# Optimization experiments

Hardware: AMD Instinct MI355X
Metric: run time of the kernel (lower is better)

Reference implementation:

```python
import math
import jax, jax.numpy as jnp
import numpy as np

B, T, C, FD, K, V = 8, 2048, 256, 256, 128, 256

def setup_inputs() -> dict:
    key = jax.random.key(0)
    ks = jax.random.split(key, 8)
    s = 0.02
    return {
        "inp": jax.random.normal(ks[0], (B, T, C), jnp.float32),
        "feature": jax.random.normal(ks[1], (B, T, FD), jnp.float32),
        "Wq": jax.random.normal(ks[2], (C + FD, K), jnp.float32) * s,
        "bq": jnp.zeros((K,), jnp.float32),
        "Wk": jax.random.normal(ks[3], (C, K), jnp.float32) * s,
        "bk": jnp.zeros((K,), jnp.float32),
        "Wv": jax.random.normal(ks[4], (C, V), jnp.float32) * s,
        "bv": jnp.zeros((V,), jnp.float32),
    }

def reference(inp, feature, Wq, bq, Wk, bk, Wv, bv):
    # inp: [B,T,C], feature: [B,T,FD]
    t = inp.shape[1]
    q = jnp.concatenate([inp, feature], axis=-1) @ Wq + bq   # [B,T,K]
    k = inp @ Wk + bk                                        # [B,T,K]
    v = inp @ Wv + bv                                        # [B,T,V]
    # scores[b, j, i] = q_j . k_i ; original masks where i > j (strict upper tri)
    scores = jnp.einsum('bjk,bik->bji', q, k)                # [B,T,T]
    mask = jnp.triu(jnp.ones((t, t), dtype=bool), k=1)       # mask[j,i] = i > j
    scores = jnp.where(mask[None], -jnp.inf, scores) / math.sqrt(K)
    # NOTE: original softmax is over dim=1 (the query/row axis), not the key axis
    attn = jax.nn.softmax(scores, axis=1)                    # [B,T,T]
    out = jnp.einsum('bji,biv->bjv', attn, v)                # [B,T,V]
    return jnp.concatenate([inp, out], axis=-1)              # [B,T,C+V]
```

## Files before the change

### kernel.cpp

```cpp
#include <hip/hip_runtime.h>
#include <hip/hip_bf16.h>
#include <cstdint>

#define Bb  8
#define Tt  2048
#define Cc  256
#define FDd 256
#define Kk  128
#define Vv  256
#define BT  (Bb * Tt)
#define NTRI 136

#define INV_SQRT_K 0.08838834764831845f

typedef __bf16 bf16x8 __attribute__((ext_vector_type(8)));
typedef __bf16 bf16x4 __attribute__((ext_vector_type(4)));
typedef float  f32x4  __attribute__((ext_vector_type(4)));

__device__ __forceinline__ void gload16(const void* g, void* l) {
  __builtin_amdgcn_global_load_lds(
      (const __attribute__((address_space(1))) void*)g,
      (__attribute__((address_space(3))) void*)l, 16, 0, 0);
}

__global__ __launch_bounds__(256) void prepw_kernel(
    const float4* __restrict__ inp4, const float4* __restrict__ feat4,
    float4* __restrict__ out4, bf16x4* __restrict__ inpB4,
    bf16x4* __restrict__ featB4,
    const float* __restrict__ Wq, const float* __restrict__ Wk,
    const float* __restrict__ Wv, __bf16* __restrict__ Wqt,
    __bf16* __restrict__ Wkt, __bf16* __restrict__ Wvt)
{
  if (blockIdx.x < 4096) {
    const int g = blockIdx.x * 256 + threadIdx.x;
    const int row = g >> 6, c = g & 63;
    const float4 x = inp4[g];
    out4[(size_t)row * 128 + c] = x;
    bf16x4 xb; xb[0] = (__bf16)x.x; xb[1] = (__bf16)x.y; xb[2] = (__bf16)x.z; xb[3] = (__bf16)x.w;
    inpB4[g] = xb;
    const float4 f = feat4[g];
    bf16x4 fb; fb[0] = (__bf16)f.x; fb[1] = (__bf16)f.y; fb[2] = (__bf16)f.z; fb[3] = (__bf16)f.w;
    featB4[g] = fb;
  } else {
    const int g = (blockIdx.x - 4096) * 256 + threadIdx.x;
    if (g < 65536) {
      const int n = g >> 9, k = g & 511;
      Wqt[g] = (__bf16)Wq[k * 128 + n];
    } else if (g < 98304) {
      const int h = g - 65536;
      const int n = h >> 8, k = h & 255;
      Wkt[h] = (__bf16)Wk[k * 128 + n];
    } else {
      const int h = g - 98304;
      const int n = h >> 8, k = h & 255;
      Wvt[h] = (__bf16)Wv[k * 256 + n];
    }
  }
}

__global__ __launch_bounds__(256, 3) void qkv_mfma_kernel(
    const __bf16* __restrict__ inpB, const __bf16* __restrict__ featB,
    const __bf16* __restrict__ Wqt, const __bf16* __restrict__ Wkt,
    const __bf16* __restrict__ Wvt,
    const float* __restrict__ bq, const float* __restrict__ bk,
    const float* __restrict__ bv,
    __bf16* __restrict__ qb, __bf16* __restrict__ kb, __bf16* __restrict__ vT)
{
  __shared__ __bf16 Atile[128 * 64];
  __shared__ __bf16 Btile[128 * 64];
  const int panel = blockIdx.y;
  const int m0 = blockIdx.x * 128;
  const int lane = threadIdx.x & 63, wave = threadIdx.x >> 6;
  const int cl = lane & 15, quad = lane >> 4;
  const int jl0 = (wave >> 1) * 64;
  const int vl0 = (wave & 1) * 64;

  const __bf16* Wt; const float* bias; int kblocks;
  if (panel == 0)      { Wt = Wqt; bias = bq; kblocks = 8; }
  else if (panel == 1) { Wt = Wkt; bias = bk; kblocks = 4; }
  else                 { Wt = Wvt + (size_t)(panel - 2) * 128 * 256;
                         bias = bv + (panel - 2) * 128; kblocks = 4; }
  const int Kd = kblocks * 64;

  const int lrow = lane >> 3;
  const int lchunk = ((lane & 7) ^ lrow) * 8;

  f32x4 acc[4][4];
#pragma unroll
  for (int mt = 0; mt < 4; ++mt)
#pragma unroll
    for (int nt = 0; nt < 4; ++nt) acc[mt][nt] = (f32x4){0.f, 0.f, 0.f, 0.f};

  for (int kb = 0; kb < kblocks; ++kb) {
    const __bf16* Asrc = (panel == 0 && kb >= 4) ? featB : inpB;
    const int koff = (panel == 0 && kb >= 4) ? (kb - 4) * 64 : kb * 64;
    __syncthreads();
#pragma unroll
    for (int t = 0; t < 4; ++t) {
      const int r0 = wave * 32 + t * 8;
      gload16(Asrc + (size_t)(m0 + r0 + lrow) * 256 + koff + lchunk, Atile + r0 * 64);
      gload16(Wt + (size_t)(r0 + lrow) * Kd + kb * 64 + lchunk, Btile + r0 * 64);
    }
    __syncthreads();
#pragma unroll
    for (int ks = 0; ks < 2; ++ks) {
      bf16x8 af[4], bfr[4];
#pragma unroll
      for (int mt = 0; mt < 4; ++mt) {
        const int jlr = jl0 + mt * 16 + cl;
        af[mt] = *(const bf16x8*)(Atile + jlr * 64 + (((ks * 4 + quad) ^ (jlr & 7)) * 8));
      }
#pragma unroll
      for (int nt = 0; nt < 4; ++nt) {
        const int vlr = vl0 + nt * 16 + cl;
        bfr[nt] = *(const bf16x8*)(Btile + vlr * 64 + (((ks * 4 + quad) ^ (vlr & 7)) * 8));
      }
#pragma unroll
      for (int mt = 0; mt < 4; ++mt)
#pragma unroll
        for (int nt = 0; nt < 4; ++nt)
          acc[mt][nt] = __builtin_amdgcn_mfma_f32_16x16x32_bf16(af[mt], bfr[nt], acc[mt][nt], 0, 0, 0);
    }
  }

  if (panel < 2) {
    __bf16* dst = (panel == 0) ? qb : kb;
    const float scale = (panel == 0) ? INV_SQRT_K : 1.0f;
#pragma unroll
    for (int mt = 0; mt < 4; ++mt) {
      const int row = m0 + jl0 + mt * 16 + quad * 4;
#pragma unroll
      for (int nt = 0; nt < 4; ++nt) {
        const int col = vl0 + nt * 16 + cl;
        const float bs = bias[col];
#pragma unroll
        for (int r = 0; r < 4; ++r)
          dst[(size_t)(row + r) * Kk + col] = (__bf16)((acc[mt][nt][r] + bs) * scale);
      }
    }
  } else {
    const int b = m0 >> 11;
#pragma unroll
    for (int mt = 0; mt < 4; ++mt) {
      const int t0 = (m0 & (Tt - 1)) + jl0 + mt * 16 + quad * 4;
#pragma unroll
      for (int nt = 0; nt < 4; ++nt) {
        const int vcol = (panel - 2) * 128 + vl0 + nt * 16 + cl;
        const float bs = bias[vl0 + nt * 16 + cl];
        bf16x4 v4;
#pragma unroll
        for (int r = 0; r < 4; ++r) v4[r] = (__bf16)(acc[mt][nt][r] + bs);
        *(bf16x4*)(vT + (size_t)(b * Vv + vcol) * Tt + t0) = v4;
      }
    }
  }
}

__global__ __launch_bounds__(256, 2) void sexp_kernel(
    const __bf16* __restrict__ qb, const __bf16* __restrict__ kb,
    __bf16* __restrict__ expS, float* __restrict__ partialD)
{
  __shared__ __bf16 tiles[2 * 128 * 128];
  __shared__ float lcs[4][64];
  __bf16* Qtile = tiles;
  __bf16* Ktile = tiles + 128 * 128;
  float*  P     = (float*)tiles;

  const int b = blockIdx.y, l = blockIdx.x;
  int jt = 0, base = 0;
  while (base + jt + 1 <= l) { base += jt + 1; ++jt; }
  const int it = l - base;

  const int lane = threadIdx.x & 63, wave = threadIdx.x >> 6;
  const int cl = lane & 15, quad = lane >> 4;
  const int jl0 = (wave >> 1) * 64;
  const int il0 = (wave & 1) * 64;
  const size_t rowbase = (size_t)b * Tt;

  {
    const int srow = lane >> 4;
    const int cslot = lane & 15;
    const __bf16* qsrc = qb + (rowbase + jt * 128) * Kk;
    const __bf16* ksrc = kb + (rowbase + it * 128) * Kk;
#pragma unroll
    for (int t = 0; t < 8; ++t) {
      const int r0 = wave * 32 + t * 4;
      const int row = r0 + srow;
      const int cg = (cslot ^ (row & 7)) * 8;
      gload16(qsrc + (size_t)row * Kk + cg, Qtile + r0 * 128);
      gload16(ksrc + (size_t)row * Kk + cg, Ktile + r0 * 128);
    }
  }
  __syncthreads();

  f32x4 acc[4][4];
#pragma unroll
  for (int mt = 0; mt < 4; ++mt)
#pragma unroll
    for (int nt = 0; nt < 4; ++nt) acc[mt][nt] = (f32x4){0.f, 0.f, 0.f, 0.f};

#pragma unroll
  for (int s = 0; s < 4; ++s) {
    bf16x8 af[4], bfr[4];
#pragma unroll
    for (int mt = 0; mt < 4; ++mt) {
      const int jlr = jl0 + mt * 16 + cl;
      af[mt] = *(const bf16x8*)(Qtile + jlr * 128 + (((s * 4 + quad) ^ (jlr & 7)) * 8));
    }
#pragma unroll
    for (int nt = 0; nt < 4; ++nt) {
      const int ilr = il0 + nt * 16 + cl;
      bfr[nt] = *(const bf16x8*)(Ktile + ilr * 128 + (((s * 4 + quad) ^ (ilr & 7)) * 8));
    }
#pragma unroll
    for (int mt = 0; mt < 4; ++mt)
#pragma unroll
      for (int nt = 0; nt < 4; ++nt)
        acc[mt][nt] = __builtin_amdgcn_mfma_f32_16x16x32_bf16(af[mt], bfr[nt], acc[mt][nt], 0, 0, 0);
  }
  __syncthreads();

  const bool diag = (it == jt);
  float cs[4] = {0.f, 0.f, 0.f, 0.f};
#pragma unroll
  for (int mt = 0; mt < 4; ++mt) {
    const int jl = jl0 + mt * 16 + quad * 4;
#pragma unroll
    for (int nt = 0; nt < 4; ++nt) {
      const int il = il0 + nt * 16 + cl;
#pragma unroll
      for (int r = 0; r < 4; ++r) {
        float p = __expf(acc[mt][nt][r]);
        if (diag && il > (jl + r)) p = 0.f;
        cs[nt] += (float)(__bf16)p;
        P[(jl + r) * 128 + il] = p;
      }
    }
  }
#pragma unroll
  for (int nt = 0; nt < 4; ++nt) {
    cs[nt] += __shfl_xor(cs[nt], 16);
    cs[nt] += __shfl_xor(cs[nt], 32);
  }
  if (quad == 0) {
#pragma unroll
    for (int nt = 0; nt < 4; ++nt) lcs[wave][nt * 16 + cl] = cs[nt];
  }
  __syncthreads();

  __bf16* slot = expS + ((size_t)(b * NTRI + l)) * (128 * 128);
  {
    const int srow = lane >> 4;
    const int c0 = (lane & 15) * 8;
#pragma unroll
    for (int t = 0; t < 8; ++t) {
      const int row = wave * 32 + t * 4 + srow;
      const f32x4 p0 = *(const f32x4*)(P + row * 128 + c0);
      const f32x4 p1 = *(const f32x4*)(P + row * 128 + c0 + 4);
      bf16x8 pb;
#pragma unroll
      for (int u = 0; u < 4; ++u) { pb[u] = (__bf16)p0[u]; pb[4 + u] = (__bf16)p1[u]; }
      *(bf16x8*)(slot + (size_t)row * 128 + c0) = pb;
    }
  }

  const int tid = threadIdx.x;
  if (tid < 128) {
    const int w0 = (tid < 64) ? 0 : 1;
    const int lc = tid & 63;
    const float s = lcs[w0][lc] + lcs[w0 + 2][lc];
    partialD[((size_t)b * 16 + jt) * Tt + it * 128 + tid] = s;
  }
}

__global__ __launch_bounds__(256) void dvscale_kernel(
    const float* __restrict__ partialD, bf16x8* __restrict__ vT8)
{
  __shared__ float rec[32];
  const int blk = blockIdx.x;
  const int b = blk >> 6, ic = blk & 63;
  const int i0 = ic * 32;
  const int tid = threadIdx.x;
  if (tid < 32) {
    const int i = i0 + tid;
    float s = 0.f;
#pragma unroll
    for (int jt = 0; jt < 16; ++jt) s += partialD[((size_t)b * 16 + jt) * Tt + i];
    rec[tid] = 1.0f / s;
  }
  __syncthreads();
  const int iu = tid & 3, v0 = tid >> 2;
#pragma unroll
  for (int p = 0; p < 4; ++p) {
    const int v = v0 + p * 64;
    const size_t idx = ((size_t)b * Vv + v) * (Tt / 8) + (i0 >> 3) + iu;
    bf16x8 x = vT8[idx];
    const int rb = iu * 8;
#pragma unroll
    for (int t = 0; t < 8; ++t) x[t] = (__bf16)((float)x[t] * rec[rb + t]);
    vT8[idx] = x;
  }
}

__global__ __launch_bounds__(512, 2) void pvgemm_kernel(
    const __bf16* __restrict__ expS, const __bf16* __restrict__ vT,
    float* __restrict__ out)
{
  __shared__ __bf16 At[2][128 * 64];
  __shared__ __bf16 Bt[2][128 * 64];
  __shared__ float red[4][16][256];
  const int b = blockIdx.y;
  const int jt = 15 - (blockIdx.x >> 1);
  const int nh = blockIdx.x & 1;
  const int tid = (int)threadIdx.x;
  const int lane = tid & 63, wave = tid >> 6;
  const int kh = wave >> 2;
  const int sq = wave & 3;
  const int cl = lane & 15, quad = lane >> 4;
  const int jl0 = (sq >> 1) * 64;
  const int vl0 = (sq & 1) * 64;

  const int nk = (jt + 1) * 2;
  const int half = nk >> 1;
  const size_t slotbase = (size_t)(b * NTRI + (jt * (jt + 1)) / 2) * 16384;
  const __bf16* vbase = vT + ((size_t)b * Vv + nh * 128) * Tt;

  const int lrow = lane >> 3;
  const int lchunk = ((lane & 7) ^ lrow) * 8;

  f32x4 acc[4][4];
#pragma unroll
  for (int mt = 0; mt < 4; ++mt)
#pragma unroll
    for (int nt = 0; nt < 4; ++nt) acc[mt][nt] = (f32x4){0.f, 0.f, 0.f, 0.f};

  for (int kbl = 0; kbl < half; ++kbl) {
    const int kb = kh * half + kbl;
    const int i0 = kb * 64;
    const __bf16* Ag = expS + slotbase + (size_t)(kb >> 1) * 16384 + (kb & 1) * 64;
    __syncthreads();
#pragma unroll
    for (int t = 0; t < 4; ++t) {
      const int r0 = sq * 32 + t * 8;
      gload16(Ag + (size_t)(r0 + lrow) * 128 + lchunk, At[kh] + r0 * 64);
      gload16(vbase + (size_t)(r0 + lrow) * Tt + i0 + lchunk, Bt[kh] + r0 * 64);
    }
    __syncthreads();
#pragma unroll
    for (int ks = 0; ks < 2; ++ks) {
      bf16x8 af[4], bfr[4];
#pragma unroll
      for (int mt = 0; mt < 4; ++mt) {
        const int jlr = jl0 + mt * 16 + cl;
        af[mt] = *(const bf16x8*)(At[kh] + jlr * 64 + (((ks * 4 + quad) ^ (jlr & 7)) * 8));
      }
#pragma unroll
      for (int nt = 0; nt < 4; ++nt) {
        const int vlr = vl0 + nt * 16 + cl;
        bfr[nt] = *(const bf16x8*)(Bt[kh] + vlr * 64 + (((ks * 4 + quad) ^ (vlr & 7)) * 8));
      }
#pragma unroll
      for (int mt = 0; mt < 4; ++mt)
#pragma unroll
        for (int nt = 0; nt < 4; ++nt)
          acc[mt][nt] = __builtin_amdgcn_mfma_f32_16x16x32_bf16(af[mt], bfr[nt], acc[mt][nt], 0, 0, 0);
    }
  }

  __syncthreads();
  if (kh == 1) {
#pragma unroll
    for (int mt = 0; mt < 4; ++mt)
#pragma unroll
      for (int nt = 0; nt < 4; ++nt)
        *(f32x4*)&red[sq][mt * 4 + nt][lane * 4] = acc[mt][nt];
  }
  __syncthreads();
  if (kh == 0) {
#pragma unroll
    for (int mt = 0; mt < 4; ++mt)
#pragma unroll
      for (int nt = 0; nt < 4; ++nt) {
        const f32x4 o = *(const f32x4*)&red[sq][mt * 4 + nt][lane * 4];
        acc[mt][nt] += o;
      }
    float* orow = out + ((size_t)b * Tt + jt * 128 + jl0) * (size_t)(Cc + Vv)
                + Cc + nh * 128 + vl0;
#pragma unroll
    for (int mt = 0; mt < 4; ++mt)
#pragma unroll
      for (int nt = 0; nt < 4; ++nt)
#pragma unroll
        for (int r = 0; r < 4; ++r)
          orow[(size_t)(mt * 16 + quad * 4 + r) * (Cc + Vv) + nt * 16 + cl] = acc[mt][nt][r];
  }
}

extern "C" void kernel_launch(void* const* d_in, const int* in_sizes, int n_in,
                              void* d_out, int out_size, void* d_ws, size_t ws_size,
                              hipStream_t stream) {
  const float* inp  = (const float*)d_in[0];
  const float* feat = (const float*)d_in[1];
  const float* Wq   = (const float*)d_in[2];
  const float* bq   = (const float*)d_in[3];
  const float* Wk   = (const float*)d_in[4];
  const float* bk   = (const float*)d_in[5];
  const float* Wv   = (const float*)d_in[6];
  const float* bv   = (const float*)d_in[7];
  float* out = (float*)d_out;

  char* ws = (char*)d_ws;
  __bf16* inpB   = (__bf16*)(ws);
  __bf16* featB  = (__bf16*)(ws + (8u << 20));
  __bf16* qb     = (__bf16*)(ws + (16u << 20));
  __bf16* kb     = (__bf16*)(ws + (20u << 20));
  __bf16* vT     = (__bf16*)(ws + (24u << 20));
  __bf16* Wqt    = (__bf16*)(ws + (32u << 20));
  __bf16* Wkt    = (__bf16*)(ws + (32u << 20) + (128u << 10));
  __bf16* Wvt    = (__bf16*)(ws + (32u << 20) + (192u << 10));
  float*  partialD = (float*)(ws + (33u << 20));
  __bf16* expS     = (__bf16*)(ws + (36u << 20));

  prepw_kernel<<<dim3(4096 + 640), 256, 0, stream>>>(
      (const float4*)inp, (const float4*)feat, (float4*)out,
      (bf16x4*)inpB, (bf16x4*)featB, Wq, Wk, Wv, Wqt, Wkt, Wvt);
  qkv_mfma_kernel<<<dim3(BT / 128, 4), 256, 0, stream>>>(
      inpB, featB, Wqt, Wkt, Wvt, bq, bk, bv, qb, kb, vT);
  sexp_kernel<<<dim3(NTRI, Bb), 256, 0, stream>>>(qb, kb, expS, partialD);
  dvscale_kernel<<<dim3(512), 256, 0, stream>>>(partialD, (bf16x8*)vT);
  pvgemm_kernel<<<dim3(32, Bb), 512, 0, stream>>>(expS, vT, out);
}
```

Before: 170.5 us.

## Recompute attention scores in PV kernel instead of materializing exp matrix

Replaces the exp-score materialization plus V-rescale pipeline with a column-sum-only pass followed by a fused kernel that recomputes QK^T, applies exp, the causal mask and the column reciprocal, and multiplies by V through an LDS tile. This removes the large bf16 expS buffer write and read and the separate dvscale launch. In exchange it doubles the QK^T compute, loads K and V fragments directly from global memory without LDS staging, and has each block redundantly reduce partialD sums.

```diff
diff --git a/kernel.cpp b/kernel.cpp
--- a/kernel.cpp
+++ b/kernel.cpp
@@ -156,16 +156,11 @@
   }
 }
 
-__global__ __launch_bounds__(256, 2) void sexp_kernel(
-    const __bf16* __restrict__ qb, const __bf16* __restrict__ kb,
-    __bf16* __restrict__ expS, float* __restrict__ partialD)
+__global__ __launch_bounds__(256, 2) void sd_kernel(
+    const __bf16* __restrict__ qb, const __bf16* __restrict__ kbuf,
+    float* __restrict__ partialD)
 {
-  __shared__ __bf16 tiles[2 * 128 * 128];
   __shared__ float lcs[4][64];
-  __bf16* Qtile = tiles;
-  __bf16* Ktile = tiles + 128 * 128;
-  float*  P     = (float*)tiles;
-
   const int b = blockIdx.y, l = blockIdx.x;
   int jt = 0, base = 0;
   while (base + jt + 1 <= l) { base += jt + 1; ++jt; }
@@ -176,22 +171,8 @@
   const int jl0 = (wave >> 1) * 64;
   const int il0 = (wave & 1) * 64;
   const size_t rowbase = (size_t)b * Tt;
-
-  {
-    const int srow = lane >> 4;
-    const int cslot = lane & 15;
-    const __bf16* qsrc = qb + (rowbase + jt * 128) * Kk;
-    const __bf16* ksrc = kb + (rowbase + it * 128) * Kk;
-#pragma unroll
-    for (int t = 0; t < 8; ++t) {
-      const int r0 = wave * 32 + t * 4;
-      const int row = r0 + srow;
-      const int cg = (cslot ^ (row & 7)) * 8;
-      gload16(qsrc + (size_t)row * Kk + cg, Qtile + r0 * 128);
-      gload16(ksrc + (size_t)row * Kk + cg, Ktile + r0 * 128);
-    }
-  }
-  __syncthreads();
+  const __bf16* qsrc = qb + (rowbase + jt * 128) * Kk;
+  const __bf16* ksrc = kbuf + (rowbase + it * 128) * Kk;
 
   f32x4 acc[4][4];
 #pragma unroll
@@ -203,22 +184,17 @@
   for (int s = 0; s < 4; ++s) {
     bf16x8 af[4], bfr[4];
 #pragma unroll
-    for (int mt = 0; mt < 4; ++mt) {
-      const int jlr = jl0 + mt * 16 + cl;
-      af[mt] = *(const bf16x8*)(Qtile + jlr * 128 + (((s * 4 + quad) ^ (jlr & 7)) * 8));
-    }
-#pragma unroll
-    for (int nt = 0; nt < 4; ++nt) {
-      const int ilr = il0 + nt * 16 + cl;
-      bfr[nt] = *(const bf16x8*)(Ktile + ilr * 128 + (((s * 4 + quad) ^ (ilr & 7)) * 8));
-    }
+    for (int mt = 0; mt < 4; ++mt)
+      af[mt] = *(const bf16x8*)(qsrc + (size_t)(jl0 + mt * 16 + cl) * Kk + (s * 4 + quad) * 8);
+#pragma unroll
+    for (int nt = 0; nt < 4; ++nt)
+      bfr[nt] = *(const bf16x8*)(ksrc + (size_t)(il0 + nt * 16 + cl) * Kk + (s * 4 + quad) * 8);
 #pragma unroll
     for (int mt = 0; mt < 4; ++mt)
 #pragma unroll
       for (int nt = 0; nt < 4; ++nt)
         acc[mt][nt] = __builtin_amdgcn_mfma_f32_16x16x32_bf16(af[mt], bfr[nt], acc[mt][nt], 0, 0, 0);
   }
-  __syncthreads();
 
   const bool diag = (it == jt);
   float cs[4] = {0.f, 0.f, 0.f, 0.f};
@@ -232,8 +208,7 @@
       for (int r = 0; r < 4; ++r) {
         float p = __expf(acc[mt][nt][r]);
         if (diag && il > (jl + r)) p = 0.f;
-        cs[nt] += (float)(__bf16)p;
-        P[(jl + r) * 128 + il] = p;
+        cs[nt] += p;
       }
     }
   }
@@ -247,22 +222,6 @@
     for (int nt = 0; nt < 4; ++nt) lcs[wave][nt * 16 + cl] = cs[nt];
   }
   __syncthreads();
-
-  __bf16* slot = expS + ((size_t)(b * NTRI + l)) * (128 * 128);
-  {
-    const int srow = lane >> 4;
-    const int c0 = (lane & 15) * 8;
-#pragma unroll
-    for (int t = 0; t < 8; ++t) {
-      const int row = wave * 32 + t * 4 + srow;
-      const f32x4 p0 = *(const f32x4*)(P + row * 128 + c0);
-      const f32x4 p1 = *(const f32x4*)(P + row * 128 + c0 + 4);
-      bf16x8 pb;
-#pragma unroll
-      for (int u = 0; u < 4; ++u) { pb[u] = (__bf16)p0[u]; pb[4 + u] = (__bf16)p1[u]; }
-      *(bf16x8*)(slot + (size_t)row * 128 + c0) = pb;
-    }
-  }
 
   const int tid = threadIdx.x;
   if (tid < 128) {
@@ -273,127 +232,114 @@
   }
 }
 
-__global__ __launch_bounds__(256) void dvscale_kernel(
-    const float* __restrict__ partialD, bf16x8* __restrict__ vT8)
-{
-  __shared__ float rec[32];
-  const int blk = blockIdx.x;
-  const int b = blk >> 6, ic = blk & 63;
-  const int i0 = ic * 32;
-  const int tid = threadIdx.x;
-  if (tid < 32) {
-    const int i = i0 + tid;
-    float s = 0.f;
-#pragma unroll
-    for (int jt = 0; jt < 16; ++jt) s += partialD[((size_t)b * 16 + jt) * Tt + i];
-    rec[tid] = 1.0f / s;
-  }
-  __syncthreads();
-  const int iu = tid & 3, v0 = tid >> 2;
-#pragma unroll
-  for (int p = 0; p < 4; ++p) {
-    const int v = v0 + p * 64;
-    const size_t idx = ((size_t)b * Vv + v) * (Tt / 8) + (i0 >> 3) + iu;
-    bf16x8 x = vT8[idx];
-    const int rb = iu * 8;
-#pragma unroll
-    for (int t = 0; t < 8; ++t) x[t] = (__bf16)((float)x[t] * rec[rb + t]);
-    vT8[idx] = x;
-  }
-}
-
-__global__ __launch_bounds__(512, 2) void pvgemm_kernel(
-    const __bf16* __restrict__ expS, const __bf16* __restrict__ vT,
+__global__ __launch_bounds__(512, 2) void pv_kernel(
+    const __bf16* __restrict__ qb, const __bf16* __restrict__ kbuf,
+    const __bf16* __restrict__ vT, const float* __restrict__ partialD,
     float* __restrict__ out)
 {
-  __shared__ __bf16 At[2][128 * 64];
-  __shared__ __bf16 Bt[2][128 * 64];
-  __shared__ float red[4][16][256];
+  __shared__ __bf16 Pt[64 * 128];
+  __shared__ float rcp[2048];
   const int b = blockIdx.y;
-  const int jt = 15 - (blockIdx.x >> 1);
-  const int nh = blockIdx.x & 1;
+  const int jt = 31 - (int)blockIdx.x;
+  const int j0 = jt * 64;
+  const int nk = (j0 >> 7) + 1;
   const int tid = (int)threadIdx.x;
   const int lane = tid & 63, wave = tid >> 6;
-  const int kh = wave >> 2;
-  const int sq = wave & 3;
   const int cl = lane & 15, quad = lane >> 4;
-  const int jl0 = (sq >> 1) * 64;
-  const int vl0 = (sq & 1) * 64;
-
-  const int nk = (jt + 1) * 2;
-  const int half = nk >> 1;
-  const size_t slotbase = (size_t)(b * NTRI + (jt * (jt + 1)) / 2) * 16384;
-  const __bf16* vbase = vT + ((size_t)b * Vv + nh * 128) * Tt;
-
-  const int lrow = lane >> 3;
-  const int lchunk = ((lane & 7) ^ lrow) * 8;
-
-  f32x4 acc[4][4];
-#pragma unroll
-  for (int mt = 0; mt < 4; ++mt)
-#pragma unroll
-    for (int nt = 0; nt < 4; ++nt) acc[mt][nt] = (f32x4){0.f, 0.f, 0.f, 0.f};
-
-  for (int kbl = 0; kbl < half; ++kbl) {
-    const int kb = kh * half + kbl;
-    const int i0 = kb * 64;
-    const __bf16* Ag = expS + slotbase + (size_t)(kb >> 1) * 16384 + (kb & 1) * 64;
+  const int wj = wave >> 2;
+  const int wi = wave & 3;
+
+  for (int i = tid; i < nk * 128; i += 512) {
+    float s = 0.f;
+#pragma unroll
+    for (int t = 0; t < 16; ++t) s += partialD[((size_t)b * 16 + t) * Tt + i];
+    rcp[i] = 1.0f / s;
+  }
+
+  const size_t rowbase = (size_t)b * Tt;
+  bf16x8 aq[2][4];
+#pragma unroll
+  for (int mt = 0; mt < 2; ++mt) {
+    const __bf16* qrow = qb + (rowbase + j0 + wj * 32 + mt * 16 + cl) * Kk;
+#pragma unroll
+    for (int s = 0; s < 4; ++s)
+      aq[mt][s] = *(const bf16x8*)(qrow + (s * 4 + quad) * 8);
+  }
+
+  f32x4 accv[2][4];
+#pragma unroll
+  for (int mt = 0; mt < 2; ++mt)
+#pragma unroll
+    for (int nt = 0; nt < 4; ++nt) accv[mt][nt] = (f32x4){0.f, 0.f, 0.f, 0.f};
+
+  __syncthreads();
+
+  const int d0 = j0 & 127;
+  for (int kbI = 0; kbI < nk; ++kbI) {
+    const int i0 = kbI * 128;
+    f32x4 aqk[2][2];
+#pragma unroll
+    for (int mt = 0; mt < 2; ++mt)
+#pragma unroll
+      for (int nt = 0; nt < 2; ++nt) aqk[mt][nt] = (f32x4){0.f, 0.f, 0.f, 0.f};
+#pragma unroll
+    for (int s = 0; s < 4; ++s) {
+      bf16x8 bk2[2];
+#pragma unroll
+      for (int nt = 0; nt < 2; ++nt)
+        bk2[nt] = *(const bf16x8*)(kbuf + (rowbase + i0 + wi * 32 + nt * 16 + cl) * Kk + (s * 4 + quad) * 8);
+#pragma unroll
+      for (int mt = 0; mt < 2; ++mt)
+#pragma unroll
+        for (int nt = 0; nt < 2; ++nt)
+          aqk[mt][nt] = __builtin_amdgcn_mfma_f32_16x16x32_bf16(aq[mt][s], bk2[nt], aqk[mt][nt], 0, 0, 0);
+    }
     __syncthreads();
-#pragma unroll
-    for (int t = 0; t < 4; ++t) {
-      const int r0 = sq * 32 + t * 8;
-      gload16(Ag + (size_t)(r0 + lrow) * 128 + lchunk, At[kh] + r0 * 64);
-      gload16(vbase + (size_t)(r0 + lrow) * Tt + i0 + lchunk, Bt[kh] + r0 * 64);
+    const bool diag = (kbI == nk - 1);
+#pragma unroll
+    for (int mt = 0; mt < 2; ++mt) {
+      const int jlb = wj * 32 + mt * 16 + quad * 4;
+#pragma unroll
+      for (int nt = 0; nt < 2; ++nt) {
+        const int il = wi * 32 + nt * 16 + cl;
+        const float r = rcp[i0 + il];
+#pragma unroll
+        for (int rr = 0; rr < 4; ++rr) {
+          float p = __expf(aqk[mt][nt][rr]);
+          if (diag && il > jlb + rr + d0) p = 0.f;
+          const int jl = jlb + rr;
+          Pt[jl * 128 + ((((il >> 3) ^ (jl & 7)) << 3) | (il & 7))] = (__bf16)(p * r);
+        }
+      }
     }
     __syncthreads();
 #pragma unroll
-    for (int ks = 0; ks < 2; ++ks) {
-      bf16x8 af[4], bfr[4];
-#pragma unroll
-      for (int mt = 0; mt < 4; ++mt) {
-        const int jlr = jl0 + mt * 16 + cl;
-        af[mt] = *(const bf16x8*)(At[kh] + jlr * 64 + (((ks * 4 + quad) ^ (jlr & 7)) * 8));
-      }
-#pragma unroll
-      for (int nt = 0; nt < 4; ++nt) {
-        const int vlr = vl0 + nt * 16 + cl;
-        bfr[nt] = *(const bf16x8*)(Bt[kh] + vlr * 64 + (((ks * 4 + quad) ^ (vlr & 7)) * 8));
-      }
-#pragma unroll
-      for (int mt = 0; mt < 4; ++mt)
+    for (int s = 0; s < 4; ++s) {
+      bf16x8 ap[2], bv4[4];
+#pragma unroll
+      for (int mt = 0; mt < 2; ++mt) {
+        const int jlr = wj * 32 + mt * 16 + cl;
+        ap[mt] = *(const bf16x8*)(Pt + jlr * 128 + (((s * 4 + quad) ^ (jlr & 7)) * 8));
+      }
+#pragma unroll
+      for (int nt = 0; nt < 4; ++nt)
+        bv4[nt] = *(const bf16x8*)(vT + ((size_t)b * Vv + wi * 64 + nt * 16 + cl) * Tt + i0 + (s * 4 + quad) * 8);
+#pragma unroll
+      for (int mt = 0; mt < 2; ++mt)
 #pragma unroll
         for (int nt = 0; nt < 4; ++nt)
-          acc[mt][nt] = __builtin_amdgcn_mfma_f32_16x16x32_bf16(af[mt], bfr[nt], acc[mt][nt], 0, 0, 0);
-    }
-  }
-
-  __syncthreads();
-  if (kh == 1) {
-#pragma unroll
-    for (int mt = 0; mt < 4; ++mt)
-#pragma unroll
-      for (int nt = 0; nt < 4; ++nt)
-        *(f32x4*)&red[sq][mt * 4 + nt][lane * 4] = acc[mt][nt];
-  }
-  __syncthreads();
-  if (kh == 0) {
-#pragma unroll
-    for (int mt = 0; mt < 4; ++mt)
-#pragma unroll
-      for (int nt = 0; nt < 4; ++nt) {
-        const f32x4 o = *(const f32x4*)&red[sq][mt * 4 + nt][lane * 4];
-        acc[mt][nt] += o;
-      }
-    float* orow = out + ((size_t)b * Tt + jt * 128 + jl0) * (size_t)(Cc + Vv)
-                + Cc + nh * 128 + vl0;
-#pragma unroll
-    for (int mt = 0; mt < 4; ++mt)
-#pragma unroll
-      for (int nt = 0; nt < 4; ++nt)
-#pragma unroll
-        for (int r = 0; r < 4; ++r)
-          orow[(size_t)(mt * 16 + quad * 4 + r) * (Cc + Vv) + nt * 16 + cl] = acc[mt][nt][r];
-  }
+          accv[mt][nt] = __builtin_amdgcn_mfma_f32_16x16x32_bf16(ap[mt], bv4[nt], accv[mt][nt], 0, 0, 0);
+    }
+  }
+
+  float* obase = out + ((size_t)b * Tt + j0 + wj * 32) * (size_t)(Cc + Vv) + Cc + wi * 64;
+#pragma unroll
+  for (int mt = 0; mt < 2; ++mt)
+#pragma unroll
+    for (int nt = 0; nt < 4; ++nt)
+#pragma unroll
+      for (int rr = 0; rr < 4; ++rr)
+        obase[(size_t)(mt * 16 + quad * 4 + rr) * (Cc + Vv) + nt * 16 + cl] = accv[mt][nt][rr];
 }
 
 extern "C" void kernel_launch(void* const* d_in, const int* in_sizes, int n_in,
@@ -419,14 +365,12 @@
   __bf16* Wkt    = (__bf16*)(ws + (32u << 20) + (128u << 10));
   __bf16* Wvt    = (__bf16*)(ws + (32u << 20) + (192u << 10));
   float*  partialD = (float*)(ws + (33u << 20));
-  __bf16* expS     = (__bf16*)(ws + (36u << 20));
 
   prepw_kernel<<<dim3(4096 + 640), 256, 0, stream>>>(
       (const float4*)inp, (const float4*)feat, (float4*)out,
       (bf16x4*)inpB, (bf16x4*)featB, Wq, Wk, Wv, Wqt, Wkt, Wvt);
   qkv_mfma_kernel<<<dim3(BT / 128, 4), 256, 0, stream>>>(
       inpB, featB, Wqt, Wkt, Wvt, bq, bk, bv, qb, kb, vT);
-  sexp_kernel<<<dim3(NTRI, Bb), 256, 0, stream>>>(qb, kb, expS, partialD);
-  dvscale_kernel<<<dim3(512), 256, 0, stream>>>(partialD, (bf16x8*)vT);
-  pvgemm_kernel<<<dim3(32, Bb), 512, 0, stream>>>(expS, vT, out);
-}
+  sd_kernel<<<dim3(NTRI, Bb), 256, 0, stream>>>(qb, kb, partialD);
+  pv_kernel<<<dim3(32, Bb), 512, 0, stream>>>(qb, kb, vT, partialD, out);
+}
```

After: 228.1 us. 33.8% more time.

## Restructure PV GEMM with paired row tiles, double buffering, and batch-major grids

Applied to the files above, without the earlier changes.

The PV GEMM kernel drops the split-K across two wave groups and its LDS reduction. Each 256-thread block now processes a complementary pair of row tiles (jt and 15-jt) over a 64-column slice of V, which balances the triangular work across blocks. It double-buffers the A and B tiles so the next k-block loads while the current one computes. The sexp, dvscale and pvgemm grids are also transposed so batch is the fastest-varying block index, which may change L2 locality. Risks are fewer blocks for the GPU's many CUs (256 PV blocks) and a longer serial k-loop per block.

```diff
diff --git a/kernel.cpp b/kernel.cpp
--- a/kernel.cpp
+++ b/kernel.cpp
@@ -166,7 +166,7 @@
   __bf16* Ktile = tiles + 128 * 128;
   float*  P     = (float*)tiles;
 
-  const int b = blockIdx.y, l = blockIdx.x;
+  const int b = blockIdx.x, l = blockIdx.y;
   int jt = 0, base = 0;
   while (base + jt + 1 <= l) { base += jt + 1; ++jt; }
   const int it = l - base;
@@ -277,8 +277,7 @@
     const float* __restrict__ partialD, bf16x8* __restrict__ vT8)
 {
   __shared__ float rec[32];
-  const int blk = blockIdx.x;
-  const int b = blk >> 6, ic = blk & 63;
+  const int b = blockIdx.x, ic = blockIdx.y;
   const int i0 = ic * 32;
   const int tid = threadIdx.x;
   if (tid < 32) {
@@ -302,94 +301,96 @@
   }
 }
 
-__global__ __launch_bounds__(512, 2) void pvgemm_kernel(
+__global__ __launch_bounds__(256, 4) void pvgemm_kernel(
     const __bf16* __restrict__ expS, const __bf16* __restrict__ vT,
     float* __restrict__ out)
 {
   __shared__ __bf16 At[2][128 * 64];
-  __shared__ __bf16 Bt[2][128 * 64];
-  __shared__ float red[4][16][256];
-  const int b = blockIdx.y;
-  const int jt = 15 - (blockIdx.x >> 1);
-  const int nh = blockIdx.x & 1;
-  const int tid = (int)threadIdx.x;
-  const int lane = tid & 63, wave = tid >> 6;
-  const int kh = wave >> 2;
-  const int sq = wave & 3;
+  __shared__ __bf16 Bt[2][64 * 64];
+  const int b = blockIdx.x;
+  const int p = blockIdx.y >> 2;
+  const int nq = blockIdx.y & 3;
+  const int lane = threadIdx.x & 63, wave = threadIdx.x >> 6;
   const int cl = lane & 15, quad = lane >> 4;
-  const int jl0 = (sq >> 1) * 64;
-  const int vl0 = (sq & 1) * 64;
-
-  const int nk = (jt + 1) * 2;
-  const int half = nk >> 1;
-  const size_t slotbase = (size_t)(b * NTRI + (jt * (jt + 1)) / 2) * 16384;
-  const __bf16* vbase = vT + ((size_t)b * Vv + nh * 128) * Tt;
-
+  const int jl0 = (wave >> 1) * 64;
+  const int vl0 = (wave & 1) * 32;
   const int lrow = lane >> 3;
   const int lchunk = ((lane & 7) ^ lrow) * 8;
-
-  f32x4 acc[4][4];
-#pragma unroll
-  for (int mt = 0; mt < 4; ++mt)
-#pragma unroll
-    for (int nt = 0; nt < 4; ++nt) acc[mt][nt] = (f32x4){0.f, 0.f, 0.f, 0.f};
-
-  for (int kbl = 0; kbl < half; ++kbl) {
-    const int kb = kh * half + kbl;
-    const int i0 = kb * 64;
-    const __bf16* Ag = expS + slotbase + (size_t)(kb >> 1) * 16384 + (kb & 1) * 64;
+  const __bf16* vbase = vT + ((size_t)b * Vv + nq * 64) * Tt;
+
+#pragma unroll
+  for (int sp = 0; sp < 2; ++sp) {
+    const int jt = sp ? p : 15 - p;
+    const int kblocks = (jt + 1) * 2;
+    const size_t slotbase = (size_t)(b * NTRI + (jt * (jt + 1)) / 2) * 16384;
+
+    f32x4 acc[4][2];
+#pragma unroll
+    for (int mt = 0; mt < 4; ++mt)
+#pragma unroll
+      for (int nt = 0; nt < 2; ++nt) acc[mt][nt] = (f32x4){0.f, 0.f, 0.f, 0.f};
+
+    {
+      const __bf16* Ag = expS + slotbase;
+#pragma unroll
+      for (int t = 0; t < 4; ++t) {
+        const int r0 = wave * 32 + t * 8;
+        gload16(Ag + (size_t)(r0 + lrow) * 128 + lchunk, At[0] + r0 * 64);
+      }
+#pragma unroll
+      for (int t = 0; t < 2; ++t) {
+        const int r0 = wave * 16 + t * 8;
+        gload16(vbase + (size_t)(r0 + lrow) * Tt + lchunk, Bt[0] + r0 * 64);
+      }
+    }
     __syncthreads();
-#pragma unroll
-    for (int t = 0; t < 4; ++t) {
-      const int r0 = sq * 32 + t * 8;
-      gload16(Ag + (size_t)(r0 + lrow) * 128 + lchunk, At[kh] + r0 * 64);
-      gload16(vbase + (size_t)(r0 + lrow) * Tt + i0 + lchunk, Bt[kh] + r0 * 64);
-    }
-    __syncthreads();
-#pragma unroll
-    for (int ks = 0; ks < 2; ++ks) {
-      bf16x8 af[4], bfr[4];
-#pragma unroll
-      for (int mt = 0; mt < 4; ++mt) {
-        const int jlr = jl0 + mt * 16 + cl;
-        af[mt] = *(const bf16x8*)(At[kh] + jlr * 64 + (((ks * 4 + quad) ^ (jlr & 7)) * 8));
-      }
-#pragma unroll
-      for (int nt = 0; nt < 4; ++nt) {
-        const int vlr = vl0 + nt * 16 + cl;
-        bfr[nt] = *(const bf16x8*)(Bt[kh] + vlr * 64 + (((ks * 4 + quad) ^ (vlr & 7)) * 8));
-      }
-#pragma unroll
-      for (int mt = 0; mt < 4; ++mt)
-#pragma unroll
-        for (int nt = 0; nt < 4; ++nt)
-          acc[mt][nt] = __builtin_amdgcn_mfma_f32_16x16x32_bf16(af[mt], bfr[nt], acc[mt][nt], 0, 0, 0);
-    }
-  }
-
-  __syncthreads();
-  if (kh == 1) {
+
+    int buf = 0;
+    for (int kb = 0; kb < kblocks; ++kb) {
+      if (kb + 1 < kblocks) {
+        const int kn = kb + 1;
+        const __bf16* Ag = expS + slotbase + (size_t)(kn >> 1) * 16384 + (kn & 1) * 64;
+        const int i0 = kn * 64;
+#pragma unroll
+        for (int t = 0; t < 4; ++t) {
+          const int r0 = wave * 32 + t * 8;
+          gload16(Ag + (size_t)(r0 + lrow) * 128 + lchunk, At[buf ^ 1] + r0 * 64);
+        }
+#pragma unroll
+        for (int t = 0; t < 2; ++t) {
+          const int r0 = wave * 16 + t * 8;
+          gload16(vbase + (size_t)(r0 + lrow) * Tt + i0 + lchunk, Bt[buf ^ 1] + r0 * 64);
+        }
+      }
+#pragma unroll
+      for (int ks = 0; ks < 2; ++ks) {
+        bf16x8 af[4], bfr[2];
+#pragma unroll
+        for (int mt = 0; mt < 4; ++mt) {
+          const int jlr = jl0 + mt * 16 + cl;
+          af[mt] = *(const bf16x8*)(At[buf] + jlr * 64 + (((ks * 4 + quad) ^ (jlr & 7)) * 8));
+        }
+#pragma unroll
+        for (int nt = 0; nt < 2; ++nt) {
+          const int vlr = vl0 + nt * 16 + cl;
+          bfr[nt] = *(const bf16x8*)(Bt[buf] + vlr * 64 + (((ks * 4 + quad) ^ (vlr & 7)) * 8));
+        }
+#pragma unroll
+        for (int mt = 0; mt < 4; ++mt)
+#pragma unroll
+          for (int nt = 0; nt < 2; ++nt)
+            acc[mt][nt] = __builtin_amdgcn_mfma_f32_16x16x32_bf16(af[mt], bfr[nt], acc[mt][nt], 0, 0, 0);
+      }
+      __syncthreads();
+      buf ^= 1;
+    }
+
+    float* orow = out + ((size_t)b * Tt + jt * 128 + jl0) * (size_t)(Cc + Vv)
+                + Cc + nq * 64 + vl0;
 #pragma unroll
     for (int mt = 0; mt < 4; ++mt)
 #pragma unroll
-      for (int nt = 0; nt < 4; ++nt)
-        *(f32x4*)&red[sq][mt * 4 + nt][lane * 4] = acc[mt][nt];
-  }
-  __syncthreads();
-  if (kh == 0) {
-#pragma unroll
-    for (int mt = 0; mt < 4; ++mt)
-#pragma unroll
-      for (int nt = 0; nt < 4; ++nt) {
-        const f32x4 o = *(const f32x4*)&red[sq][mt * 4 + nt][lane * 4];
-        acc[mt][nt] += o;
-      }
-    float* orow = out + ((size_t)b * Tt + jt * 128 + jl0) * (size_t)(Cc + Vv)
-                + Cc + nh * 128 + vl0;
-#pragma unroll
-    for (int mt = 0; mt < 4; ++mt)
-#pragma unroll
-      for (int nt = 0; nt < 4; ++nt)
+      for (int nt = 0; nt < 2; ++nt)
 #pragma unroll
         for (int r = 0; r < 4; ++r)
           orow[(size_t)(mt * 16 + quad * 4 + r) * (Cc + Vv) + nt * 16 + cl] = acc[mt][nt][r];
@@ -426,7 +427,7 @@
       (bf16x4*)inpB, (bf16x4*)featB, Wq, Wk, Wv, Wqt, Wkt, Wvt);
   qkv_mfma_kernel<<<dim3(BT / 128, 4), 256, 0, stream>>>(
       inpB, featB, Wqt, Wkt, Wvt, bq, bk, bv, qb, kb, vT);
-  sexp_kernel<<<dim3(NTRI, Bb), 256, 0, stream>>>(qb, kb, expS, partialD);
-  dvscale_kernel<<<dim3(512), 256, 0, stream>>>(partialD, (bf16x8*)vT);
-  pvgemm_kernel<<<dim3(32, Bb), 512, 0, stream>>>(expS, vT, out);
-}
+  sexp_kernel<<<dim3(Bb, NTRI), 256, 0, stream>>>(qb, kb, expS, partialD);
+  dvscale_kernel<<<dim3(Bb, 64), 256, 0, stream>>>(partialD, (bf16x8*)vT);
+  pvgemm_kernel<<<dim3(Bb, 32), 256, 0, stream>>>(expS, vT, out);
+}
```

New measurement: 160.1 us. 6.1% less time.
